# Kernel tuning notes

Hardware: AMD Instinct MI355X
Metric: run time of the kernel (lower is better)

The kernel has to match this reference:

```python
import jax, jax.numpy as jnp
import numpy as np

C = 384          # input_channels
DH = 768         # dim_hidden
WS = 7           # window size (kernel_size)
NH = 12          # num_heads
HID = 3072       # mlp hidden = dim_hidden * mlp_ratio
NP = WS * WS     # 49 patch tokens
N = NP + 1       # + 1 cls token
SCALE = (C // NH) ** -0.5
REL_DIM = 2 * WS - 1


def _rel_pos_index():
    r = np.arange(WS)
    qx, qy = np.meshgrid(r, r, indexing='ij')
    q = np.stack([qx.ravel(), qy.ravel()], -1)                 # [NP,2], row-major flatten
    rel = q[:, None, :] - q[None, :, :] + WS - 1               # [NP,NP,2], values in [0,2ws-2]
    return jnp.asarray(rel[..., 0] * REL_DIM + rel[..., 1])    # [NP,NP]

REL_IDX = _rel_pos_index()


def layer_norm(x, g, b, eps=1e-5):
    m = jnp.mean(x, axis=-1, keepdims=True)
    v = jnp.var(x, axis=-1, keepdims=True)
    return (x - m) * jax.lax.rsqrt(v + eps) * g + b


def attention(x, w_qkv, w_proj, b_proj, rel_pos=None, mask=None):
    Bx, Nx, Cx = x.shape
    qkv = (x @ w_qkv.T).reshape(Bx, Nx, 3, NH, Cx // NH).transpose(2, 0, 3, 1, 4)
    q, k, v = qkv[0], qkv[1], qkv[2]                           # [B,H,N,d]
    attn = jnp.einsum('bhqd,bhkd->bhqk', q, k) * SCALE
    if rel_pos is not None:
        bias = rel_pos[REL_IDX].transpose(2, 0, 1)[None]       # [1,NH,NP,NP]
        attn = attn.at[:, :, 1:, 1:].add(bias)                 # skip cls token row/col
    if mask is not None:
        attn = attn + mask[:, None]                            # broadcast over heads
    attn = jax.nn.softmax(attn, axis=-1)
    y = jnp.einsum('bhqk,bhkd->bhqd', attn, v).transpose(0, 2, 1, 3).reshape(Bx, Nx, Cx)
    return y @ w_proj.T + b_proj


def setup_inputs() -> dict:
    key = jax.random.key(0)
    ks = jax.random.split(key, 16)
    s = 0.02
    BNW = 2048  # B * num_windows = 32 * 64
    return {
        'out': jax.random.normal(ks[0], (BNW, N, C), jnp.float32),
        'mask': jnp.zeros((BNW, N, N), jnp.float32),
        'g0': jnp.ones((C,), jnp.float32), 'b0': jnp.zeros((C,), jnp.float32),
        'g1': jnp.ones((C,), jnp.float32), 'b1': jnp.zeros((C,), jnp.float32),
        'g2': jnp.ones((C,), jnp.float32), 'b2': jnp.zeros((C,), jnp.float32),
        'ge': jnp.ones((C,), jnp.float32), 'be': jnp.zeros((C,), jnp.float32),
        'w_qkv': jax.random.normal(ks[1], (3 * C, C), jnp.float32) * s,
        'w_proj': jax.random.normal(ks[2], (C, C), jnp.float32) * s,
        'b_proj': jnp.zeros((C,), jnp.float32),
        'rel_pos': jax.random.normal(ks[3], (REL_DIM * REL_DIM, NH), jnp.float32) * s,
        'w_fc1': jax.random.normal(ks[4], (HID, C), jnp.float32) * s,
        'b_fc1': jnp.zeros((HID,), jnp.float32),
        'w_fc2': jax.random.normal(ks[5], (DH, HID), jnp.float32) * s,
        'b_fc2': jnp.zeros((DH,), jnp.float32),
        'w_exp': jax.random.normal(ks[6], (DH, C), jnp.float32) * s,
        'b_exp': jnp.zeros((DH,), jnp.float32),
        'w_lin': jax.random.normal(ks[7], (C, DH), jnp.float32) * s,
        'b_lin': jnp.zeros((C,), jnp.float32),
        'B': 32, 'H': 56, 'W': 56,
    }


def reference(out, mask, g0, b0, g1, b1, g2, b2, ge, be,
              w_qkv, w_proj, b_proj, rel_pos,
              w_fc1, b_fc1, w_fc2, b_fc2, w_exp, b_exp, w_lin, b_lin,
              B, H, W):
    Cc = out.shape[-1]
    # cls-token attention across windows of each image
    cls = out[:, :1].reshape(B, -1, Cc)                        # [B, nw, C]
    cls = cls + attention(layer_norm(cls, g0, b0), w_qkv, w_proj, b_proj)
    cls = cls.reshape(-1, 1, Cc)
    x = jnp.concatenate([cls, out[:, 1:]], axis=1)             # [B*nw, N, C]
    # windowed patch attention with rel-pos bias + mask
    x = x + attention(layer_norm(x, g1, b1), w_qkv, w_proj, b_proj,
                      rel_pos=rel_pos, mask=mask)
    # expand path: norm -> gelu -> linear (input_channels != dim_hidden)
    identity = jax.nn.gelu(layer_norm(x, ge, be), approximate=False) @ w_exp.T + b_exp
    # mlp path: norm -> fc1 -> gelu -> fc2
    h = layer_norm(x, g2, b2)
    h = jax.nn.gelu(h @ w_fc1.T + b_fc1, approximate=False)
    h = h @ w_fc2.T + b_fc2
    tmp = identity + h                                          # [B*nw, N, DH]
    return tmp @ w_lin.T + b_lin                                # [B*nw, N, C]
```

## Files before the change

kernel.cpp:

```cpp
#include <hip/hip_runtime.h>
#include <hip/hip_bf16.h>
#include <math.h>

#define NHEADS 12
#define NTOK   50
#define NWIN   2048
#define IMGS   32
#define CDIM   384
#define QKVD   1152
#define DHID   768
#define MLPH   3072
#define KTAIL  3456
#define SCALE_F 0.17677669529663687f

typedef short short8 __attribute__((ext_vector_type(8)));
typedef short short4v __attribute__((ext_vector_type(4)));
typedef short short2v __attribute__((ext_vector_type(2)));
typedef float f32x4  __attribute__((ext_vector_type(4)));
typedef __hip_bfloat16 bf16;

__device__ __forceinline__ float gelu_f(float x){
  float z = 0.7978845608028654f*(x + 0.044715f*x*x*x);
  float e = __expf(2.0f*z);
  return 0.5f*x*(1.0f + (1.0f - 2.0f/(e+1.0f)));
}
__device__ __forceinline__ float gelu_fast(float x){
  float e = __expf(-1.702f*x);
  return x / (1.0f + e);
}
__device__ __forceinline__ short bfs(float x){
  bf16 h = __float2bfloat16(x); return *(short*)&h;
}

__global__ void cvt4_kernel(const float* s0, bf16* d0, int n0,
                            const float* s1, bf16* d1, int n1,
                            const float* s2, bf16* d2, int n2,
                            const float* s3, bf16* d3, int n3){
  int stride = gridDim.x*blockDim.x, g = blockIdx.x*blockDim.x + threadIdx.x;
  for (int i=g; i<n0; i+=stride) d0[i] = __float2bfloat16(s0[i]);
  for (int i=g; i<n1; i+=stride) d1[i] = __float2bfloat16(s1[i]);
  for (int i=g; i<n2; i+=stride) d2[i] = __float2bfloat16(s2[i]);
  for (int i=g; i<n3; i+=stride) d3[i] = __float2bfloat16(s3[i]);
}

__global__ __launch_bounds__(256) void transpose_cvt_kernel(const float* __restrict__ src,
    bf16* __restrict__ dst, int R, int Cc){
  __shared__ float tile[32][33];
  int bx = blockIdx.x, by = blockIdx.y;
  int c = threadIdx.x & 31, r0 = threadIdx.x >> 5;
  #pragma unroll
  for (int rr = r0; rr < 32; rr += 8)
    tile[rr][c] = src[(size_t)(by*32+rr)*Cc + bx*32 + c];
  __syncthreads();
  #pragma unroll
  for (int rr = r0; rr < 32; rr += 8)
    dst[(size_t)(bx*32+rr)*R + by*32 + c] = __float2bfloat16(tile[c][rr]);
}

__global__ void bias_combine_kernel(const float* __restrict__ wlin,
    const float* __restrict__ b_lin, const float* __restrict__ b_exp,
    const float* __restrict__ b_fc2, float* __restrict__ biasc){
  int i = blockIdx.x*blockDim.x + threadIdx.x;
  if (i >= CDIM) return;
  float s = b_lin[i];
  for (int d=0; d<DHID; d++) s += wlin[(size_t)i*DHID+d]*(b_exp[d]+b_fc2[d]);
  biasc[i] = s;
}

template<bool GELU>
__global__ __launch_bounds__(256) void ln_kernel(const float* __restrict__ x, long ldx,
    const float* __restrict__ g, const float* __restrict__ b,
    bf16* __restrict__ y, int rows)
{
  int row = blockIdx.x*4 + (threadIdx.x>>6);
  if (row >= rows) return;
  int l = threadIdx.x & 63;
  const float2* xr = (const float2*)(x + (size_t)row*ldx);
  float2 v[3]; float s = 0.f;
  #pragma unroll
  for (int j=0;j<3;j++){ v[j] = xr[l + 64*j]; s += v[j].x + v[j].y; }
  #pragma unroll
  for (int off=32; off; off>>=1) s += __shfl_xor(s, off, 64);
  float mean = s * (1.0f/384.0f);
  float vs = 0.f;
  #pragma unroll
  for (int j=0;j<3;j++){ float dx=v[j].x-mean, dy=v[j].y-mean; vs += dx*dx+dy*dy; }
  #pragma unroll
  for (int off=32; off; off>>=1) vs += __shfl_xor(vs, off, 64);
  float rstd = rsqrtf(vs*(1.0f/384.0f) + 1e-5f);
  short2v* yr = (short2v*)(y + (size_t)row*384);
  const float2* gv = (const float2*)g; const float2* bv = (const float2*)b;
  #pragma unroll
  for (int j=0;j<3;j++){
    float2 gg = gv[l+64*j], bb = bv[l+64*j];
    float o0 = (v[j].x-mean)*rstd*gg.x + bb.x;
    float o1 = (v[j].y-mean)*rstd*gg.y + bb.y;
    if (GELU){ o0 = gelu_f(o0); o1 = gelu_f(o1); }
    short2v pk; pk[0]=bfs(o0); pk[1]=bfs(o1);
    yr[l+64*j] = pk;
  }
}

__global__ __launch_bounds__(256) void ln_dual_kernel(const float* __restrict__ x,
    const float* __restrict__ ge, const float* __restrict__ be,
    const float* __restrict__ g2, const float* __restrict__ b2,
    bf16* __restrict__ yeo, long lde, bf16* __restrict__ y2o, int rows)
{
  int row = blockIdx.x*4 + (threadIdx.x>>6);
  if (row >= rows) return;
  int l = threadIdx.x & 63;
  const float2* xr = (const float2*)(x + (size_t)row*384);
  float2 v[3]; float s = 0.f;
  #pragma unroll
  for (int j=0;j<3;j++){ v[j] = xr[l + 64*j]; s += v[j].x + v[j].y; }
  #pragma unroll
  for (int off=32; off; off>>=1) s += __shfl_xor(s, off, 64);
  float mean = s * (1.0f/384.0f);
  float vs = 0.f;
  #pragma unroll
  for (int j=0;j<3;j++){ float dx=v[j].x-mean, dy=v[j].y-mean; vs += dx*dx+dy*dy; }
  #pragma unroll
  for (int off=32; off; off>>=1) vs += __shfl_xor(vs, off, 64);
  float rstd = rsqrtf(vs*(1.0f/384.0f) + 1e-5f);
  short2v* ye = (short2v*)(yeo + (size_t)row*lde);
  short2v* y2 = (short2v*)(y2o + (size_t)row*384);
  const float2* gev = (const float2*)ge; const float2* bev = (const float2*)be;
  const float2* g2v = (const float2*)g2; const float2* b2v = (const float2*)b2;
  #pragma unroll
  for (int j=0;j<3;j++){
    float n0 = (v[j].x-mean)*rstd, n1 = (v[j].y-mean)*rstd;
    float2 gg = gev[l+64*j], bb = bev[l+64*j];
    short2v pe; pe[0]=bfs(gelu_f(n0*gg.x+bb.x)); pe[1]=bfs(gelu_f(n1*gg.y+bb.y));
    ye[l+64*j] = pe;
    gg = g2v[l+64*j]; bb = b2v[l+64*j];
    short2v p2; p2[0]=bfs(n0*gg.x+bb.x); p2[1]=bfs(n1*gg.y+bb.y);
    y2[l+64*j] = p2;
  }
}

template<bool OUT_BF16, bool BIAS, int RES, int GELU>
__device__ __forceinline__ void gemm_dev(
    const bf16* __restrict__ A, const bf16* __restrict__ B, void* Cv,
    const float* __restrict__ bias, const void* res,
    int M, int N, int K, int ldc, int ldres)
{
  __shared__ short As[3][128*32];
  __shared__ short Bs[3][128*32];
  const int t  = threadIdx.x;
  const int l  = t & 63;
  const int w  = t >> 6;
  const int wr = w >> 1, wc = w & 1;
  const int lr = l & 15, kg = l >> 4;

  const int nwg = gridDim.x * gridDim.y;
  const int lin = blockIdx.y * gridDim.x + blockIdx.x;
  const int q8 = nwg >> 3, r8 = nwg & 7;
  const int xcd = lin & 7, slot = lin >> 3;
  const int swz = (xcd < r8) ? (xcd*(q8+1) + slot) : (r8*(q8+1) + (xcd-r8)*q8 + slot);
  const int by = swz / gridDim.x, bx = swz - by*gridDim.x;

  const int bm = by * 128, bn = bx * 128;
  const short* Ag = (const short*)A;
  const short* Bg = (const short*)B;

  const int eo0 = w*1024 + l*8;
  const int rowS0 = eo0 >> 5, colS0 = eo0 & 31;
  const int eo1 = eo0 + 512;
  const int rowS1 = eo1 >> 5, colS1 = eo1 & 31;

  #define STAGE(k0, b) do { \
    __builtin_amdgcn_global_load_lds( \
      (const __attribute__((address_space(1))) void*)&Ag[(size_t)(bm+rowS0)*K + (k0) + colS0], \
      (__attribute__((address_space(3))) void*)((char*)&As[b][0] + w*2048), 16, 0, 0); \
    __builtin_amdgcn_global_load_lds( \
      (const __attribute__((address_space(1))) void*)&Bg[(size_t)(bn+rowS0)*K + (k0) + colS0], \
      (__attribute__((address_space(3))) void*)((char*)&Bs[b][0] + w*2048), 16, 0, 0); \
    __builtin_amdgcn_global_load_lds( \
      (const __attribute__((address_space(1))) void*)&Ag[(size_t)(bm+rowS1)*K + (k0) + colS1], \
      (__attribute__((address_space(3))) void*)((char*)&As[b][0] + w*2048 + 1024), 16, 0, 0); \
    __builtin_amdgcn_global_load_lds( \
      (const __attribute__((address_space(1))) void*)&Bg[(size_t)(bn+rowS1)*K + (k0) + colS1], \
      (__attribute__((address_space(3))) void*)((char*)&Bs[b][0] + w*2048 + 1024), 16, 0, 0); \
  } while(0)

  f32x4 acc[4][4] = {};

  STAGE(0, 0);
  STAGE(32, 1);
  asm volatile("s_waitcnt vmcnt(4)" ::: "memory");
  __builtin_amdgcn_s_barrier();

  int cur = 0, nb = 2;
  for (int k0 = 0; k0 < K; k0 += 32) {
    const bool more = (k0 + 64 < K);
    if (more) STAGE(k0 + 64, nb);

    short8 af[4], bfm[4];
    #pragma unroll
    for (int m=0;m<4;m++) af[m]  = *(const short8*)(&As[cur][(wr*64 + m*16 + lr)*32 + kg*8]);
    #pragma unroll
    for (int n=0;n<4;n++) bfm[n] = *(const short8*)(&Bs[cur][(wc*64 + n*16 + lr)*32 + kg*8]);
    __builtin_amdgcn_s_setprio(1);
    #pragma unroll
    for (int m=0;m<4;m++)
      #pragma unroll
      for (int n=0;n<4;n++)
        acc[m][n] = __builtin_amdgcn_mfma_f32_16x16x32_bf16(af[m], bfm[n], acc[m][n], 0,0,0);
    __builtin_amdgcn_s_setprio(0);

    if (more) { asm volatile("s_waitcnt vmcnt(4)" ::: "memory"); }
    else      { asm volatile("s_waitcnt vmcnt(0)" ::: "memory"); }
    __builtin_amdgcn_s_barrier();
    cur = (cur==2) ? 0 : cur+1;
    nb  = (nb==2)  ? 0 : nb+1;
  }
  #undef STAGE

  #pragma unroll
  for (int m=0;m<4;m++){
    int row0 = bm + wr*64 + m*16 + kg*4;
    #pragma unroll
    for (int n=0;n<4;n++){
      int col = bn + wc*64 + n*16 + lr;
      float bv = BIAS ? bias[col] : 0.0f;
      #pragma unroll
      for (int r=0;r<4;r++){
        float val = acc[m][n][r] + bv;
        if (RES == 1) val += ((const float*)res)[(size_t)(row0+r)*ldres + col];
        if (GELU == 1) val = gelu_fast(val);
        if (OUT_BF16) ((bf16*)Cv)[(size_t)(row0+r)*ldc + col] = __float2bfloat16(val);
        else          ((float*)Cv)[(size_t)(row0+r)*ldc + col] = val;
      }
    }
  }
}

#define GEMM_K(NAME, OB, BI, RE, GE) \
__global__ __launch_bounds__(256) void NAME( \
    const bf16* __restrict__ A, const bf16* __restrict__ B, void* Cv, \
    const float* __restrict__ bias, const void* res, \
    int M, int N, int K, int ldc, int ldres){ \
  gemm_dev<OB,BI,RE,GE>(A,B,Cv,bias,res,M,N,K,ldc,ldres); }

GEMM_K(gemm_qkv_k,  true,  false, 0, 0)
GEMM_K(gemm_proj_k, false, true,  1, 0)
GEMM_K(gemm_fc1_k,  true,  true,  0, 1)
GEMM_K(gemm_tail_k, false, true,  0, 0)
GEMM_K(gemm_wcmb_k, true,  false, 0, 0)

__global__ __launch_bounds__(256) void attn_cls_kernel(const bf16* __restrict__ qkv,
                                                       bf16* __restrict__ y)
{
  int img = blockIdx.x, h = blockIdx.y;
  __shared__ float q[64][33], k[64][33], v[64][33];
  __shared__ float s[64][65];
  int t = threadIdx.x;
  for (int idx=t; idx<64*32; idx+=256){
    int i = idx>>5, d = idx&31;
    const bf16* base = qkv + ((size_t)(img*64+i))*QKVD + h*32 + d;
    q[i][d] = __bfloat162float(base[0]);
    k[i][d] = __bfloat162float(base[384]);
    v[i][d] = __bfloat162float(base[768]);
  }
  __syncthreads();
  for (int idx=t; idx<64*64; idx+=256){
    int i = idx>>6, j = idx&63;
    float a = 0.f;
    #pragma unroll
    for (int d=0; d<32; d++) a += q[i][d]*k[j][d];
    s[i][j] = a * SCALE_F;
  }
  __syncthreads();
  if (t < 64){
    float m = -1e30f;
    for (int j=0;j<64;j++) m = fmaxf(m, s[t][j]);
    float sum = 0.f;
    for (int j=0;j<64;j++){ float e = __expf(s[t][j]-m); s[t][j]=e; sum+=e; }
    float inv = 1.0f/sum;
    for (int j=0;j<64;j++) s[t][j] *= inv;
  }
  __syncthreads();
  for (int idx=t; idx<64*32; idx+=256){
    int i = idx>>5, d = idx&31;
    float a = 0.f;
    for (int j=0;j<64;j++) a += s[i][j]*v[j][d];
    y[((size_t)(img*64+i))*CDIM + h*32 + d] = __float2bfloat16(a);
  }
}

__global__ __launch_bounds__(64) void attn_win_mfma(const bf16* __restrict__ qkv,
    const float* __restrict__ mask, const float* __restrict__ rel_pos,
    bf16* __restrict__ y)
{
  const int lw = blockIdx.x, h = blockIdx.y;
  const int l = threadIdx.x;
  const int lr = l & 15, kg = l >> 4;
  __shared__ short Plds[64*72];
  __shared__ short VTl[32*72];
  __shared__ float rp[169];

  const size_t tok0 = (size_t)lw * NTOK;
  const short* qbase = (const short*)qkv;

  for (int i=l; i<169; i+=64) rp[i] = rel_pos[i*NHEADS + h];

  short8 qf[4], kf[4];
  #pragma unroll
  for (int n=0;n<4;n++){
    int qt = 16*n + lr;
    if (qt < 50) qf[n] = *(const short8*)&qbase[(tok0+qt)*QKVD + h*32 + kg*8];
    else         qf[n] = short8(0);
  }
  #pragma unroll
  for (int m=0;m<4;m++){
    int kt = 16*m + lr;
    if (kt < 50) kf[m] = *(const short8*)&qbase[(tok0+kt)*QKVD + 384 + h*32 + kg*8];
    else         kf[m] = short8(0);
  }

  {
    short vv[32];
    if (l < 50){
      const short8* vp = (const short8*)&qbase[(tok0+l)*QKVD + 768 + h*32];
      #pragma unroll
      for (int jj=0;jj<4;jj++){ short8 xv = vp[jj];
        #pragma unroll
        for (int e=0;e<8;e++) vv[jj*8+e] = xv[e]; }
    } else {
      #pragma unroll
      for (int d=0; d<32; d++) vv[d]=0;
    }
    #pragma unroll
    for (int d=0; d<32; d++) VTl[d*72 + l] = vv[d];
  }

  f32x4 sacc[4][4] = {};
  #pragma unroll
  for (int m=0;m<4;m++)
    #pragma unroll
    for (int n=0;n<4;n++)
      sacc[m][n] = __builtin_amdgcn_mfma_f32_16x16x32_bf16(kf[m], qf[n], sacc[m][n], 0,0,0);

  const float* mrow = mask + (size_t)lw*2500;
  float sv[4][4][4];
  #pragma unroll
  for (int m=0;m<4;m++){
    #pragma unroll
    for (int r=0;r<4;r++){
      int kt = 16*m + 4*kg + r;
      #pragma unroll
      for (int n=0;n<4;n++){
        int qt = 16*n + lr;
        float a;
        if (kt < 50 && qt < 50){
          a = sacc[m][n][r] * SCALE_F;
          if (kt>=1 && qt>=1){
            int qi=qt-1, kj=kt-1;
            int ridx = ((qi/7)-(kj/7)+6)*13 + (qi%7)-(kj%7)+6;
            a += rp[ridx];
          }
          a += mrow[qt*50+kt];
        } else a = -1e30f;
        sv[m][r][n] = a;
      }
    }
  }

  #pragma unroll
  for (int n=0;n<4;n++){
    float mx = -1e30f;
    #pragma unroll
    for (int m=0;m<4;m++)
      #pragma unroll
      for (int r=0;r<4;r++) mx = fmaxf(mx, sv[m][r][n]);
    mx = fmaxf(mx, __shfl_xor(mx, 16));
    mx = fmaxf(mx, __shfl_xor(mx, 32));
    float sum = 0.f;
    float pv[4][4];
    #pragma unroll
    for (int m=0;m<4;m++)
      #pragma unroll
      for (int r=0;r<4;r++){ float p = __expf(sv[m][r][n]-mx); pv[m][r]=p; sum+=p; }
    sum += __shfl_xor(sum, 16);
    sum += __shfl_xor(sum, 32);
    float inv = 1.0f/sum;
    int qrow = (16*n + lr)*72;
    #pragma unroll
    for (int m=0;m<4;m++){
      short4v pk;
      #pragma unroll
      for (int r=0;r<4;r++) pk[r] = bfs(pv[m][r]*inv);
      *(short4v*)&Plds[qrow + 16*m + 4*kg] = pk;
    }
  }
  __syncthreads();

  f32x4 oacc[2][4] = {};
  #pragma unroll
  for (int ks=0; ks<2; ks++){
    short8 pf[4];
    #pragma unroll
    for (int n=0;n<4;n++)
      pf[n] = *(const short8*)&Plds[(16*n+lr)*72 + 32*ks + kg*8];
    #pragma unroll
    for (int md=0; md<2; md++){
      short8 vf = *(const short8*)&VTl[(16*md+lr)*72 + 32*ks + kg*8];
      #pragma unroll
      for (int n=0;n<4;n++)
        oacc[md][n] = __builtin_amdgcn_mfma_f32_16x16x32_bf16(vf, pf[n], oacc[md][n], 0,0,0);
    }
  }

  short* yb = (short*)y;
  #pragma unroll
  for (int n=0;n<4;n++){
    int qt = 16*n + lr;
    if (qt >= 50) continue;
    #pragma unroll
    for (int md=0; md<2; md++){
      short4v pk;
      #pragma unroll
      for (int r=0;r<4;r++) pk[r] = bfs(oacc[md][n][r]);
      *(short4v*)&yb[(tok0+qt)*CDIM + h*32 + 16*md + 4*kg] = pk;
    }
  }
}

extern "C" void kernel_launch(void* const* d_in, const int* in_sizes, int n_in,
                              void* d_out, int out_size, void* d_ws, size_t ws_size,
                              hipStream_t stream)
{
  const float* x_in   = (const float*)d_in[0];
  const float* maskp  = (const float*)d_in[1];
  const float* g0 = (const float*)d_in[2];  const float* b0 = (const float*)d_in[3];
  const float* g1 = (const float*)d_in[4];  const float* b1 = (const float*)d_in[5];
  const float* g2 = (const float*)d_in[6];  const float* b2 = (const float*)d_in[7];
  const float* ge = (const float*)d_in[8];  const float* be = (const float*)d_in[9];
  const float* w_qkv = (const float*)d_in[10];
  const float* w_proj= (const float*)d_in[11];
  const float* b_proj= (const float*)d_in[12];
  const float* rel_pos=(const float*)d_in[13];
  const float* w_fc1 = (const float*)d_in[14];
  const float* b_fc1 = (const float*)d_in[15];
  const float* w_fc2 = (const float*)d_in[16];
  const float* b_fc2 = (const float*)d_in[17];
  const float* w_exp = (const float*)d_in[18];
  const float* b_exp = (const float*)d_in[19];
  const float* w_lin = (const float*)d_in[20];
  const float* b_lin = (const float*)d_in[21];
  float* dout = (float*)d_out;

  const size_t NT = (size_t)NWIN * NTOK;

  size_t off = 0;
  auto alloc = [&](size_t bytes)->void* {
    void* p = (char*)d_ws + off;
    off += (bytes + 255) & ~(size_t)255;
    return p;
  };

  bf16* wqkv_b = (bf16*)alloc((size_t)QKVD*CDIM*2);
  bf16* wproj_b= (bf16*)alloc((size_t)CDIM*CDIM*2);
  bf16* wfc1_b = (bf16*)alloc((size_t)MLPH*CDIM*2);
  bf16* wlin_b = (bf16*)alloc((size_t)CDIM*DHID*2);
  bf16* wexpT_b= (bf16*)alloc((size_t)CDIM*DHID*2);
  bf16* wfc2T_b= (bf16*)alloc((size_t)MLPH*DHID*2);
  bf16* W_comb = (bf16*)alloc((size_t)CDIM*KTAIL*2);
  float* biasc = (float*)alloc((size_t)CDIM*4);
  float* xb    = (float*)alloc(NT*CDIM*4);
  bf16* clsln  = (bf16*)alloc((size_t)NWIN*CDIM*2);
  bf16* qkvcls = (bf16*)alloc((size_t)NWIN*QKVD*2);
  bf16* ycls   = (bf16*)alloc((size_t)NWIN*CDIM*2);

  int CH_W = 2048;
  const size_t per_window = 537600ull;
  while (CH_W > 128 && off + (size_t)CH_W*per_window + 16384 > ws_size) CH_W >>= 1;
  const int CH_T = CH_W * NTOK;

  bf16*  xln   = (bf16*) alloc((size_t)CH_T*CDIM*2);
  bf16*  qkvc  = (bf16*) alloc((size_t)CH_T*QKVD*2);
  bf16*  ybfc  = (bf16*) alloc((size_t)CH_T*CDIM*2);
  bf16*  h1ext = (bf16*) alloc((size_t)CH_T*KTAIL*2);

  cvt4_kernel<<<512, 256, 0, stream>>>(
      w_qkv, wqkv_b, QKVD*CDIM,  w_proj, wproj_b, CDIM*CDIM,
      w_fc1, wfc1_b, MLPH*CDIM,  w_lin,  wlin_b,  CDIM*DHID);
  transpose_cvt_kernel<<<dim3(CDIM/32, DHID/32), 256, 0, stream>>>(w_exp, wexpT_b, DHID, CDIM);
  transpose_cvt_kernel<<<dim3(MLPH/32, DHID/32), 256, 0, stream>>>(w_fc2, wfc2T_b, DHID, MLPH);
  bias_combine_kernel<<<6, 64, 0, stream>>>(w_lin, b_lin, b_exp, b_fc2, biasc);
  gemm_wcmb_k<<<dim3(CDIM/128, CDIM/128), 256, 0, stream>>>(
      wlin_b, wexpT_b, W_comb, nullptr, nullptr, CDIM, CDIM, DHID, KTAIL, 0);
  gemm_wcmb_k<<<dim3(MLPH/128, CDIM/128), 256, 0, stream>>>(
      wlin_b, wfc2T_b, W_comb + 384, nullptr, nullptr, CDIM, MLPH, DHID, KTAIL, 0);

  hipMemcpyAsync(xb, x_in, NT*CDIM*4, hipMemcpyDeviceToDevice, stream);

  ln_kernel<false><<<NWIN/4, 256, 0, stream>>>(x_in, (long)NTOK*CDIM, g0, b0, clsln, NWIN);
  gemm_qkv_k<<<dim3(QKVD/128, NWIN/128), 256, 0, stream>>>(
      clsln, wqkv_b, qkvcls, nullptr, nullptr, NWIN, QKVD, CDIM, QKVD, 0);
  attn_cls_kernel<<<dim3(IMGS, NHEADS), 256, 0, stream>>>(qkvcls, ycls);
  gemm_proj_k<<<dim3(CDIM/128, NWIN/128), 256, 0, stream>>>(
      ycls, wproj_b, xb, b_proj, x_in, NWIN, CDIM, CDIM, NTOK*CDIM, NTOK*CDIM);

  const int nch = NWIN / CH_W;
  for (int c = 0; c < nch; c++){
    int w0 = c * CH_W;
    size_t t0 = (size_t)w0 * NTOK;
    float* xbc = xb + t0*CDIM;
    float* doutc = dout + t0*CDIM;
    int MT = CH_T, MB = CH_T/128;

    ln_kernel<false><<<MT/4, 256, 0, stream>>>(xbc, CDIM, g1, b1, xln, MT);
    gemm_qkv_k<<<dim3(QKVD/128, MB), 256, 0, stream>>>(
        xln, wqkv_b, qkvc, nullptr, nullptr, MT, QKVD, CDIM, QKVD, 0);
    attn_win_mfma<<<dim3(CH_W, NHEADS), 64, 0, stream>>>(
        qkvc, maskp + (size_t)w0*2500, rel_pos, ybfc);
    gemm_proj_k<<<dim3(CDIM/128, MB), 256, 0, stream>>>(
        ybfc, wproj_b, xbc, b_proj, xbc, MT, CDIM, CDIM, CDIM, CDIM);

    ln_dual_kernel<<<MT/4, 256, 0, stream>>>(xbc, ge, be, g2, b2, h1ext, KTAIL, ybfc, MT);

    gemm_fc1_k<<<dim3(MLPH/128, MB), 256, 0, stream>>>(
        ybfc, wfc1_b, h1ext + 384, b_fc1, nullptr, MT, MLPH, CDIM, KTAIL, 0);

    gemm_tail_k<<<dim3(CDIM/128, MB), 256, 0, stream>>>(
        h1ext, W_comb, doutc, biasc, nullptr, MT, CDIM, KTAIL, CDIM, 0);
  }
}
```

Before: 1.778 ms.

## Split tail GEMM along K into two halves with a separate reduce kernel

The final tail GEMM (K=3456, N=384) now runs split-K with two K segments via a third grid dimension. Each segment writes an fp32 partial into a scratch buffer that reuses the xln/qkvc workspace. A new reduce kernel sums the two partials, adds the combined bias and writes the output. The GEMM device function gains separate lda/ldb strides to support this. The aim is more workgroups per GEMM, at the cost of extra global traffic from writing and re-reading two full fp32 partial matrices, and the reliance on aliased scratch memory being large enough.

```diff
diff --git a/kernel.cpp b/kernel.cpp
--- a/kernel.cpp
+++ b/kernel.cpp
@@ -67,6 +67,19 @@
   biasc[i] = s;
 }
 
+__global__ __launch_bounds__(256) void sk_reduce_kernel(
+    const float4* __restrict__ p0, const float4* __restrict__ p1,
+    const float4* __restrict__ bc, float4* __restrict__ out, int n)
+{
+  for (int i = blockIdx.x*blockDim.x + threadIdx.x; i < n; i += gridDim.x*blockDim.x){
+    float4 x = p0[i], y = p1[i], z = bc[i % 96];
+    float4 r;
+    r.x = x.x + y.x + z.x;  r.y = x.y + y.y + z.y;
+    r.z = x.z + y.z + z.z;  r.w = x.w + y.w + z.w;
+    out[i] = r;
+  }
+}
+
 template<bool GELU>
 __global__ __launch_bounds__(256) void ln_kernel(const float* __restrict__ x, long ldx,
     const float* __restrict__ g, const float* __restrict__ b,
@@ -142,7 +155,7 @@
 __device__ __forceinline__ void gemm_dev(
     const bf16* __restrict__ A, const bf16* __restrict__ B, void* Cv,
     const float* __restrict__ bias, const void* res,
-    int M, int N, int K, int ldc, int ldres)
+    int M, int N, int K, int lda, int ldb, int ldc, int ldres)
 {
   __shared__ short As[3][128*32];
   __shared__ short Bs[3][128*32];
@@ -170,16 +183,16 @@
 
   #define STAGE(k0, b) do { \
     __builtin_amdgcn_global_load_lds( \
-      (const __attribute__((address_space(1))) void*)&Ag[(size_t)(bm+rowS0)*K + (k0) + colS0], \
+      (const __attribute__((address_space(1))) void*)&Ag[(size_t)(bm+rowS0)*lda + (k0) + colS0], \
       (__attribute__((address_space(3))) void*)((char*)&As[b][0] + w*2048), 16, 0, 0); \
     __builtin_amdgcn_global_load_lds( \
-      (const __attribute__((address_space(1))) void*)&Bg[(size_t)(bn+rowS0)*K + (k0) + colS0], \
+      (const __attribute__((address_space(1))) void*)&Bg[(size_t)(bn+rowS0)*ldb + (k0) + colS0], \
       (__attribute__((address_space(3))) void*)((char*)&Bs[b][0] + w*2048), 16, 0, 0); \
     __builtin_amdgcn_global_load_lds( \
-      (const __attribute__((address_space(1))) void*)&Ag[(size_t)(bm+rowS1)*K + (k0) + colS1], \
+      (const __attribute__((address_space(1))) void*)&Ag[(size_t)(bm+rowS1)*lda + (k0) + colS1], \
       (__attribute__((address_space(3))) void*)((char*)&As[b][0] + w*2048 + 1024), 16, 0, 0); \
     __builtin_amdgcn_global_load_lds( \
-      (const __attribute__((address_space(1))) void*)&Bg[(size_t)(bn+rowS1)*K + (k0) + colS1], \
+      (const __attribute__((address_space(1))) void*)&Bg[(size_t)(bn+rowS1)*ldb + (k0) + colS1], \
       (__attribute__((address_space(3))) void*)((char*)&Bs[b][0] + w*2048 + 1024), 16, 0, 0); \
   } while(0)
 
@@ -239,14 +252,23 @@
 __global__ __launch_bounds__(256) void NAME( \
     const bf16* __restrict__ A, const bf16* __restrict__ B, void* Cv, \
     const float* __restrict__ bias, const void* res, \
-    int M, int N, int K, int ldc, int ldres){ \
-  gemm_dev<OB,BI,RE,GE>(A,B,Cv,bias,res,M,N,K,ldc,ldres); }
+    int M, int N, int K, int lda, int ldc, int ldres){ \
+  gemm_dev<OB,BI,RE,GE>(A,B,Cv,bias,res,M,N,K,lda,K,ldc,ldres); }
 
 GEMM_K(gemm_qkv_k,  true,  false, 0, 0)
 GEMM_K(gemm_proj_k, false, true,  1, 0)
 GEMM_K(gemm_fc1_k,  true,  true,  0, 1)
-GEMM_K(gemm_tail_k, false, true,  0, 0)
 GEMM_K(gemm_wcmb_k, true,  false, 0, 0)
+
+__global__ __launch_bounds__(256) void gemm_tail_sk(
+    const bf16* __restrict__ A, const bf16* __restrict__ B, float* part,
+    int M)
+{
+  const int seg = blockIdx.z;
+  gemm_dev<false,false,0,0>(
+      A + seg*(KTAIL/2), B + seg*(KTAIL/2), part + (size_t)seg*M*CDIM,
+      nullptr, nullptr, M, CDIM, KTAIL/2, KTAIL, KTAIL, CDIM, 0);
+}
 
 __global__ __launch_bounds__(256) void attn_cls_kernel(const bf16* __restrict__ qkv,
                                                        bf16* __restrict__ y)
@@ -481,6 +503,7 @@
   bf16*  qkvc  = (bf16*) alloc((size_t)CH_T*QKVD*2);
   bf16*  ybfc  = (bf16*) alloc((size_t)CH_T*CDIM*2);
   bf16*  h1ext = (bf16*) alloc((size_t)CH_T*KTAIL*2);
+  float* skpart = (float*)xln;
 
   cvt4_kernel<<<512, 256, 0, stream>>>(
       w_qkv, wqkv_b, QKVD*CDIM,  w_proj, wproj_b, CDIM*CDIM,
@@ -489,18 +512,18 @@
   transpose_cvt_kernel<<<dim3(MLPH/32, DHID/32), 256, 0, stream>>>(w_fc2, wfc2T_b, DHID, MLPH);
   bias_combine_kernel<<<6, 64, 0, stream>>>(w_lin, b_lin, b_exp, b_fc2, biasc);
   gemm_wcmb_k<<<dim3(CDIM/128, CDIM/128), 256, 0, stream>>>(
-      wlin_b, wexpT_b, W_comb, nullptr, nullptr, CDIM, CDIM, DHID, KTAIL, 0);
+      wlin_b, wexpT_b, W_comb, nullptr, nullptr, CDIM, CDIM, DHID, DHID, KTAIL, 0);
   gemm_wcmb_k<<<dim3(MLPH/128, CDIM/128), 256, 0, stream>>>(
-      wlin_b, wfc2T_b, W_comb + 384, nullptr, nullptr, CDIM, MLPH, DHID, KTAIL, 0);
+      wlin_b, wfc2T_b, W_comb + 384, nullptr, nullptr, CDIM, MLPH, DHID, DHID, KTAIL, 0);
 
   hipMemcpyAsync(xb, x_in, NT*CDIM*4, hipMemcpyDeviceToDevice, stream);
 
   ln_kernel<false><<<NWIN/4, 256, 0, stream>>>(x_in, (long)NTOK*CDIM, g0, b0, clsln, NWIN);
   gemm_qkv_k<<<dim3(QKVD/128, NWIN/128), 256, 0, stream>>>(
-      clsln, wqkv_b, qkvcls, nullptr, nullptr, NWIN, QKVD, CDIM, QKVD, 0);
+      clsln, wqkv_b, qkvcls, nullptr, nullptr, NWIN, QKVD, CDIM, CDIM, QKVD, 0);
   attn_cls_kernel<<<dim3(IMGS, NHEADS), 256, 0, stream>>>(qkvcls, ycls);
   gemm_proj_k<<<dim3(CDIM/128, NWIN/128), 256, 0, stream>>>(
-      ycls, wproj_b, xb, b_proj, x_in, NWIN, CDIM, CDIM, NTOK*CDIM, NTOK*CDIM);
+      ycls, wproj_b, xb, b_proj, x_in, NWIN, CDIM, CDIM, CDIM, NTOK*CDIM, NTOK*CDIM);
 
   const int nch = NWIN / CH_W;
   for (int c = 0; c < nch; c++){
@@ -512,18 +535,21 @@
 
     ln_kernel<false><<<MT/4, 256, 0, stream>>>(xbc, CDIM, g1, b1, xln, MT);
     gemm_qkv_k<<<dim3(QKVD/128, MB), 256, 0, stream>>>(
-        xln, wqkv_b, qkvc, nullptr, nullptr, MT, QKVD, CDIM, QKVD, 0);
+        xln, wqkv_b, qkvc, nullptr, nullptr, MT, QKVD, CDIM, CDIM, QKVD, 0);
     attn_win_mfma<<<dim3(CH_W, NHEADS), 64, 0, stream>>>(
         qkvc, maskp + (size_t)w0*2500, rel_pos, ybfc);
     gemm_proj_k<<<dim3(CDIM/128, MB), 256, 0, stream>>>(
-        ybfc, wproj_b, xbc, b_proj, xbc, MT, CDIM, CDIM, CDIM, CDIM);
+        ybfc, wproj_b, xbc, b_proj, xbc, MT, CDIM, CDIM, CDIM, CDIM, CDIM);
 
     ln_dual_kernel<<<MT/4, 256, 0, stream>>>(xbc, ge, be, g2, b2, h1ext, KTAIL, ybfc, MT);
 
     gemm_fc1_k<<<dim3(MLPH/128, MB), 256, 0, stream>>>(
-        ybfc, wfc1_b, h1ext + 384, b_fc1, nullptr, MT, MLPH, CDIM, KTAIL, 0);
-
-    gemm_tail_k<<<dim3(CDIM/128, MB), 256, 0, stream>>>(
-        h1ext, W_comb, doutc, biasc, nullptr, MT, CDIM, KTAIL, CDIM, 0);
-  }
-}
+        ybfc, wfc1_b, h1ext + 384, b_fc1, nullptr, MT, MLPH, CDIM, CDIM, KTAIL, 0);
+
+    gemm_tail_sk<<<dim3(CDIM/128, MB, 2), 256, 0, stream>>>(
+        h1ext, W_comb, skpart, MT);
+    sk_reduce_kernel<<<2048, 256, 0, stream>>>(
+        (const float4*)skpart, (const float4*)(skpart + (size_t)MT*CDIM),
+        (const float4*)biasc, (float4*)doutc, MT*CDIM/4);
+  }
+}
```

After: 1.952 ms. 9.8% more time.
